# Kernel tuning notes

Hardware: AMD Instinct MI355X
Metric: run time of the kernel (lower is better)

The kernel has to match this reference:

```python
import jax, jax.numpy as jnp
import numpy as np

BITS = 8
NUM_HEADS = 16
EMB = 1024
MLP = 4096
BATCH = 4
SEQ = 1024


def _fq(x, bits, signed=True, narrow=False):
    """Fake-quantize with per-tensor absmax scale (brevitas MinMax/MaxStats style),
    straight-through-estimator round. signed+narrow => weight quant; signed non-narrow
    => activation quant; unsigned => QuantReLU output."""
    if signed:
        qmax = 2.0 ** (bits - 1) - 1.0
        qmin = -qmax if narrow else -(qmax + 1.0)
    else:
        qmax = 2.0 ** bits - 1.0
        qmin = 0.0
    scale = jax.lax.stop_gradient(jnp.max(jnp.abs(x)) / qmax)
    scale = jnp.maximum(scale, jnp.asarray(1e-8, x.dtype))
    q = x / scale
    q = q + jax.lax.stop_gradient(jnp.round(q) - q)  # STE round
    return jnp.clip(q, qmin, qmax) * scale


def _layernorm(x, eps=1e-5):
    mu = jnp.mean(x, axis=-1, keepdims=True)
    var = jnp.mean(jnp.square(x - mu), axis=-1, keepdims=True)
    return (x - mu) * jax.lax.rsqrt(var + eps)


def setup_inputs() -> dict:
    key = jax.random.key(0)
    ks = jax.random.split(key, 11)
    def w(k, shape, fan_in):
        return jax.random.normal(k, shape, jnp.float32) * (1.0 / np.sqrt(fan_in))
    return {
        "x": jax.random.normal(ks[0], (BATCH, SEQ, EMB), jnp.float32),
        "Wq": w(ks[1], (EMB, EMB), EMB), "bq": jnp.zeros((EMB,), jnp.float32),
        "Wk": w(ks[2], (EMB, EMB), EMB), "bk": jnp.zeros((EMB,), jnp.float32),
        "Wv": w(ks[3], (EMB, EMB), EMB), "bv": jnp.zeros((EMB,), jnp.float32),
        "Wo": w(ks[4], (EMB, EMB), EMB), "bo": jnp.zeros((EMB,), jnp.float32),
        "W1": w(ks[5], (MLP, EMB), EMB), "b1": jnp.zeros((MLP,), jnp.float32),
        "W2": w(ks[6], (EMB, MLP), MLP), "b2": jnp.zeros((EMB,), jnp.float32),
    }


def reference(x, Wq, bq, Wk, bk, Wv, bv, Wo, bo, W1, b1, W2, b2):
    B, S, E = x.shape
    H, D = NUM_HEADS, EMB // NUM_HEADS
    fqw = lambda W: _fq(W, BITS, signed=True, narrow=True)   # weight quant
    fqb = lambda b: _fq(b, BITS, signed=True)                # bias quant
    fqa = lambda a: _fq(a, BITS, signed=True)                # act quant

    # sdp_input_quant
    qx = fqa(x)
    # separate (unpacked) in-projections, torch Linear: y = x @ W.T + b
    q = qx @ fqw(Wq).T + fqb(bq)
    k = qx @ fqw(Wk).T + fqb(bk)
    v = qx @ fqw(Wv).T + fqb(bv)
    # [B,H,S,D]
    q = q.reshape(B, S, H, D).transpose(0, 2, 1, 3)
    k = k.reshape(B, S, H, D).transpose(0, 2, 1, 3)
    v = v.reshape(B, S, H, D).transpose(0, 2, 1, 3)

    q_scaled = fqa(q * (1.0 / np.sqrt(D)))          # q_scaled_quant
    k_t = fqa(k.transpose(0, 1, 3, 2))              # k_transposed_quant
    v = fqa(v)                                      # v_quant

    scores = jnp.einsum('bhqd,bhdk->bhqk', q_scaled, k_t)
    scores = fqa(scores)                            # softmax_input_quant
    attn = jax.nn.softmax(scores, axis=-1)
    attn = fqa(attn)                                # attn_output_weights_quant

    ctx = jnp.einsum('bhqk,bhkd->bhqd', attn, v)
    ctx = ctx.transpose(0, 2, 1, 3).reshape(B, S, E)
    ctx = fqa(ctx)                                  # out_proj_input_quant
    attn_out = ctx @ fqw(Wo).T + fqb(bo)

    # residual_sdp (QuantEltwiseAdd input quant on both operands) + layer-norm
    h = _layernorm(fqa(x) + fqa(attn_out))

    # MLP: QuantIdentity -> QuantLinear -> QuantReLU(unsigned) -> QuantLinear
    m = fqa(h)
    m = m @ fqw(W1).T + fqb(b1)
    m = _fq(jax.nn.relu(m), BITS, signed=False)
    m = m @ fqw(W2).T + fqb(b2)

    return _layernorm(fqa(h) + fqa(m))
```

## Files before the change

kernel.cpp:

```cpp
#include <hip/hip_runtime.h>
#include <cstdint>
#include <cstddef>

#define TB_B 4
#define TB_S 1024
#define TB_E 1024
#define TB_H 16
#define TB_D 64
#define TB_MLP 4096
#define TB_ROWS (TB_B * TB_S)

typedef int int4v __attribute__((ext_vector_type(4)));

#define LGKM0() __asm__ volatile("s_waitcnt lgkmcnt(0)" ::: "memory")
#define CMEMBAR() __asm__ volatile("" ::: "memory")
#define RAW_BARRIER() do { __asm__ volatile("" ::: "memory"); \
  __builtin_amdgcn_s_barrier(); __asm__ volatile("" ::: "memory"); } while (0)

static __device__ __forceinline__ void atomicMaxF(float* addr, float v) {
  atomicMax(reinterpret_cast<unsigned int*>(addr), __float_as_uint(v));
}

static __device__ __forceinline__ float fast_exp2(float x) {
#if __has_builtin(__builtin_amdgcn_exp2f)
  return __builtin_amdgcn_exp2f(x);
#else
  return exp2f(x);
#endif
}

static __device__ __forceinline__ void gl2lds16(const void* g, void* l) {
  __builtin_amdgcn_global_load_lds(
      (const __attribute__((address_space(1))) void*)g,
      (__attribute__((address_space(3))) void*)l, 16, 0, 0);
}

struct AMDesc { const float* p; long n4; int slot; };
struct AMBatch { AMDesc d[13]; };
__global__ __launch_bounds__(256) void absmax_multi_kernel(AMBatch bt, float* ws) {
  AMDesc d = bt.d[blockIdx.y];
  float m = 0.f;
  long stride = (long)gridDim.x * 256;
  for (long i = (long)blockIdx.x * 256 + threadIdx.x; i < d.n4; i += stride) {
    float4 v = ((const float4*)d.p)[i];
    m = fmaxf(m, fmaxf(fmaxf(fabsf(v.x), fabsf(v.y)), fmaxf(fabsf(v.z), fabsf(v.w))));
  }
#pragma unroll
  for (int o = 32; o; o >>= 1) m = fmaxf(m, __shfl_down(m, o, 64));
  __shared__ float sm[4];
  if (!(threadIdx.x & 63)) sm[threadIdx.x >> 6] = m;
  __syncthreads();
  if (threadIdx.x == 0)
    atomicMaxF(ws + d.slot, fmaxf(fmaxf(sm[0], sm[1]), fmaxf(sm[2], sm[3])));
}

struct QMDesc { const float* in; signed char* out; long n4; int slot; float qmin; };
struct QMBatch { QMDesc d[7]; };
__global__ __launch_bounds__(256) void quant8_multi_kernel(QMBatch bt, const float* ws) {
  QMDesc d = bt.d[blockIdx.y];
  float scale = fmaxf(ws[d.slot] / 127.f, 1e-8f);
  long stride = (long)gridDim.x * 256;
  for (long i = (long)blockIdx.x * 256 + threadIdx.x; i < d.n4; i += stride) {
    float4 v = ((const float4*)d.in)[i];
    char4 o;
    o.x = (signed char)(int)fminf(fmaxf(rintf(v.x / scale), d.qmin), 127.f);
    o.y = (signed char)(int)fminf(fmaxf(rintf(v.y / scale), d.qmin), 127.f);
    o.z = (signed char)(int)fminf(fmaxf(rintf(v.z / scale), d.qmin), 127.f);
    o.w = (signed char)(int)fminf(fmaxf(rintf(v.w / scale), d.qmin), 127.f);
    ((char4*)d.out)[i] = o;
  }
}

struct BDesc { const float* in; float* out; int n4; int slot; };
struct BBatch { BDesc d[6]; };
__global__ __launch_bounds__(256) void bias_quant_multi_kernel(BBatch bt, const float* ws) {
  BDesc d = bt.d[blockIdx.y];
  float scale = fmaxf(ws[d.slot] / 127.f, 1e-8f);
  int i = blockIdx.x * 256 + threadIdx.x;
  if (i < d.n4) {
    float4 v = ((const float4*)d.in)[i];
    float4 o;
    o.x = fminf(fmaxf(rintf(v.x / scale), -128.f), 127.f) * scale;
    o.y = fminf(fmaxf(rintf(v.y / scale), -128.f), 127.f) * scale;
    o.z = fminf(fmaxf(rintf(v.z / scale), -128.f), 127.f) * scale;
    o.w = fminf(fmaxf(rintf(v.w / scale), -128.f), 127.f) * scale;
    ((float4*)d.out)[i] = o;
  }
}

__global__ __launch_bounds__(256) void quant8_kernel(const float* __restrict__ in,
                                                     signed char* __restrict__ out8, long n4,
                                                     const float* __restrict__ amax_p,
                                                     float pre, float qmin) {
  float scale = fmaxf(amax_p[0] * pre / 127.f, 1e-8f);
  long stride = (long)gridDim.x * 256;
  for (long i = (long)blockIdx.x * 256 + threadIdx.x; i < n4; i += stride) {
    float4 v = ((const float4*)in)[i];
    char4 o;
    o.x = (signed char)(int)fminf(fmaxf(rintf(v.x * pre / scale), qmin), 127.f);
    o.y = (signed char)(int)fminf(fmaxf(rintf(v.y * pre / scale), qmin), 127.f);
    o.z = (signed char)(int)fminf(fmaxf(rintf(v.z * pre / scale), qmin), 127.f);
    o.w = (signed char)(int)fminf(fmaxf(rintf(v.w * pre / scale), qmin), 127.f);
    ((char4*)out8)[i] = o;
  }
}

__global__ __launch_bounds__(256) void relu_quant8_kernel(const float* __restrict__ in,
                                                          signed char* __restrict__ out8, long n4,
                                                          const float* __restrict__ amax_p) {
  float scale = fmaxf(amax_p[0] / 255.f, 1e-8f);
  long stride = (long)gridDim.x * 256;
  for (long i = (long)blockIdx.x * 256 + threadIdx.x; i < n4; i += stride) {
    float4 v = ((const float4*)in)[i];
    char4 o;
    o.x = (signed char)((int)fminf(fmaxf(rintf(fmaxf(v.x, 0.f) / scale), 0.f), 255.f) - 128);
    o.y = (signed char)((int)fminf(fmaxf(rintf(fmaxf(v.y, 0.f) / scale), 0.f), 255.f) - 128);
    o.z = (signed char)((int)fminf(fmaxf(rintf(fmaxf(v.z, 0.f) / scale), 0.f), 255.f) - 128);
    o.w = (signed char)((int)fminf(fmaxf(rintf(fmaxf(v.w, 0.f) / scale), 0.f), 255.f) - 128);
    ((char4*)out8)[i] = o;
  }
}

__global__ __launch_bounds__(256) void rowsum_i8_kernel(const signed char* __restrict__ w8,
                                                        int* __restrict__ out, int Kdim) {
  const int row = blockIdx.x, t = threadIdx.x;
  const signed char* p = w8 + (long)row * Kdim;
  int s = 0;
  for (int i = t * 16; i < Kdim; i += 4096) {
    int4v v = *(const int4v*)(p + i);
    const signed char* b = (const signed char*)&v;
#pragma unroll
    for (int j = 0; j < 16; j++) s += b[j];
  }
#pragma unroll
  for (int o = 32; o; o >>= 1) s += __shfl_down(s, o, 64);
  __shared__ int sm[4];
  if (!(t & 63)) sm[t >> 6] = s;
  __syncthreads();
  if (t == 0) out[row] = sm[0] + sm[1] + sm[2] + sm[3];
}

__global__ __launch_bounds__(256) void gemm_i8_kernel(
    const signed char* __restrict__ A, const signed char* __restrict__ Bw,
    const float* __restrict__ biasq,
    const float* __restrict__ amax_a, float div_a,
    const float* __restrict__ amax_b,
    const int* __restrict__ rowsum,
    float* __restrict__ C, int M, int N, int K,
    float* __restrict__ amax_out, int relu_amax, int mode) {
  __shared__ signed char As[3][8192];
  __shared__ signed char Bs[3][8192];
  const int t = threadIdx.x;
  int bx, by;
  {
    int lin = blockIdx.y * gridDim.x + blockIdx.x;
    if ((gridDim.y & 7) == 0) {
      int xcd = lin & 7, j = lin >> 3;
      bx = j % gridDim.x;
      by = (gridDim.y >> 3) * xcd + j / gridDim.x;
    } else { bx = blockIdx.x; by = blockIdx.y; }
  }
  const int m0 = by * 128, n0 = bx * 128;
  const int w = t >> 6, lane = t & 63;
  const int fr = lane & 15, quad = lane >> 4;
  const int wm = w >> 1, wn = w & 1;
  const int r0 = t >> 2;
  const int csrc = (((t & 3) ^ ((t >> 3) & 3)) << 4);
  const int sx = ((quad ^ ((fr >> 1) & 3)) << 4);

  int4v acc[4][4];
#pragma unroll
  for (int r = 0; r < 4; r++)
#pragma unroll
    for (int c = 0; c < 4; c++) acc[r][c] = (int4v){0, 0, 0, 0};

  const long arow0 = (long)(m0 + r0) * K + csrc;
  const long arow1 = (long)(m0 + r0 + 64) * K + csrc;
  const long brow0 = (long)(n0 + r0) * K + csrc;
  const long brow1 = (long)(n0 + r0 + 64) * K + csrc;

  auto stage = [&](int buf, int kt) {
    const int kk = kt << 6;
    gl2lds16(A + arow0 + kk, As[buf] + t * 16);
    gl2lds16(A + arow1 + kk, As[buf] + t * 16 + 4096);
    gl2lds16(Bw + brow0 + kk, Bs[buf] + t * 16);
    gl2lds16(Bw + brow1 + kk, Bs[buf] + t * 16 + 4096);
  };
  auto compute = [&](int buf) {
    int4v af[4], bf[4];
#pragma unroll
    for (int r = 0; r < 4; r++)
      af[r] = *(const int4v*)(As[buf] + (wm * 64 + r * 16 + fr) * 64 + sx);
#pragma unroll
    for (int c = 0; c < 4; c++)
      bf[c] = *(const int4v*)(Bs[buf] + (wn * 64 + c * 16 + fr) * 64 + sx);
#pragma unroll
    for (int r = 0; r < 4; r++)
#pragma unroll
      for (int c = 0; c < 4; c++)
        acc[r][c] = __builtin_amdgcn_mfma_i32_16x16x64_i8(af[r], bf[c], acc[r][c], 0, 0, 0);
  };

  const int nt = K >> 6;
  stage(0, 0);
  stage(1, 1);
  int cbuf = 0, sbuf = 2;
  for (int kt = 0; kt < nt - 1; ++kt) {
    __asm__ volatile("s_waitcnt vmcnt(4)" ::: "memory");
    RAW_BARRIER();
    if (kt + 2 < nt) { stage(sbuf, kt + 2); sbuf = (sbuf == 2) ? 0 : sbuf + 1; }
    compute(cbuf);
    cbuf = (cbuf == 2) ? 0 : cbuf + 1;
  }
  __asm__ volatile("s_waitcnt vmcnt(0)" ::: "memory");
  RAW_BARRIER();
  compute(cbuf);

  const int seg = (mode == 1) ? (n0 >> 10) : 0;
  const float s_a = fmaxf(amax_a[0] / div_a, 1e-8f);
  const float s_b = fmaxf(amax_b[seg] / 127.f, 1e-8f);
  const float s = s_a * s_b;
  float lmax = 0.f;
#pragma unroll
  for (int r = 0; r < 4; r++) {
    int rbase = m0 + wm * 64 + r * 16 + quad * 4;
#pragma unroll
    for (int c = 0; c < 4; c++) {
      int col = n0 + wn * 64 + c * 16 + fr;
      int corr = rowsum ? (rowsum[col] << 7) : 0;
      float bi = biasq[col];
      if (mode == 1) {
        int h = (col >> 6) & 15, dd = col & 63;
        float* cbase = C + (long)seg * ((long)TB_ROWS * TB_E);
#pragma unroll
        for (int g = 0; g < 4; g++) {
          int m = rbase + g;
          int b = m >> 10, sdx = m & 1023;
          float o = (float)acc[r][c][g] * s + bi;
          lmax = fmaxf(lmax, fabsf(o));
          cbase[((((long)b * TB_H + h) * TB_S) + sdx) * TB_D + dd] = o;
        }
      } else {
#pragma unroll
        for (int g = 0; g < 4; g++) {
          float o = (float)(acc[r][c][g] + corr) * s + bi;
          lmax = fmaxf(lmax, relu_amax ? fmaxf(o, 0.f) : fabsf(o));
          C[(long)(rbase + g) * N + col] = o;
        }
      }
    }
  }
#pragma unroll
  for (int o = 32; o; o >>= 1) lmax = fmaxf(lmax, __shfl_down(lmax, o, 64));
  __shared__ float redm[4];
  if (!lane) redm[w] = lmax;
  __syncthreads();
  if (t == 0) atomicMaxF(amax_out + seg, fmaxf(fmaxf(redm[0], redm[1]), fmaxf(redm[2], redm[3])));
}

__global__ __launch_bounds__(256) void quant8_vb_kernel(const float* __restrict__ v,
                                                        const float* __restrict__ amax_p,
                                                        signed char* __restrict__ v8b) {
  __shared__ signed char tile[64][80];
  const int bh = blockIdx.x;
  const int jb = blockIdx.y;
  const int s0 = jb * 64;
  const int t = threadIdx.x;
  const float scale = fmaxf(amax_p[0] / 127.f, 1e-8f);
#pragma unroll
  for (int it = 0; it < 4; it++) {
    int idx = t + it * 256;
    int r = idx >> 4, c4 = (idx & 15) * 4;
    float4 vv = *(const float4*)(v + ((long)bh * TB_S + s0 + r) * TB_D + c4);
    tile[c4 + 0][r] = (signed char)(int)fminf(fmaxf(rintf(vv.x / scale), -128.f), 127.f);
    tile[c4 + 1][r] = (signed char)(int)fminf(fmaxf(rintf(vv.y / scale), -128.f), 127.f);
    tile[c4 + 2][r] = (signed char)(int)fminf(fmaxf(rintf(vv.z / scale), -128.f), 127.f);
    tile[c4 + 3][r] = (signed char)(int)fminf(fmaxf(rintf(vv.w / scale), -128.f), 127.f);
  }
  __syncthreads();
  int d = t >> 2, sb = (t & 3) * 16;
  int4v o = *(const int4v*)&tile[d][sb];
  *(int4v*)(v8b + (((long)bh * 16 + jb) * 64 + d) * 64 + sb) = o;
}

__global__ __launch_bounds__(256) void attn_rowmax_kernel(const signed char* __restrict__ q8,
                                                          const signed char* __restrict__ k8,
                                                          int* __restrict__ irowmax,
                                                          int* __restrict__ imax_out) {
  const int bh = blockIdx.x;
  const int t = threadIdx.x, w = t >> 6, lane = t & 63;
  const int fr = lane & 15, quad = lane >> 4;
  const int i0 = blockIdx.y * 64 + w * 16;
  const long base = (long)bh * TB_S;
  int4v qf = *(const int4v*)(q8 + (base + i0 + fr) * 64 + quad * 16);
  int mx = -2147483647, mn = 2147483647;
  for (int j0 = 0; j0 < TB_S; j0 += 16) {
    int4v kf = *(const int4v*)(k8 + (base + j0 + fr) * 64 + quad * 16);
    int4v sc = __builtin_amdgcn_mfma_i32_16x16x64_i8(kf, qf, (int4v){0, 0, 0, 0}, 0, 0, 0);
    mx = max(mx, max(max(sc[0], sc[1]), max(sc[2], sc[3])));
    mn = min(mn, min(min(sc[0], sc[1]), min(sc[2], sc[3])));
  }
  mx = max(mx, __shfl_xor(mx, 16, 64));
  mx = max(mx, __shfl_xor(mx, 32, 64));
  mn = min(mn, __shfl_xor(mn, 16, 64));
  mn = min(mn, __shfl_xor(mn, 32, 64));
  if (quad == 0) irowmax[(long)bh * TB_S + i0 + fr] = mx;
  int gm = max(mx, -mn);
#pragma unroll
  for (int o = 32; o; o >>= 1) gm = max(gm, __shfl_down(gm, o, 64));
  __shared__ int sm[4];
  if (!lane) sm[w] = gm;
  __syncthreads();
  if (t == 0) atomicMax(imax_out, max(max(sm[0], sm[1]), max(sm[2], sm[3])));
}

__global__ __launch_bounds__(256) void attn_rowsum_kernel(
    const signed char* __restrict__ q8, const signed char* __restrict__ k8,
    const int* __restrict__ irowmax, const int* __restrict__ imax_p,
    const float* __restrict__ amax_q, const float* __restrict__ amax_k,
    float* __restrict__ rowl, float* __restrict__ amax_attn) {
  const int bh = blockIdx.x;
  const int t = threadIdx.x, w = t >> 6, lane = t & 63;
  const int fr = lane & 15, quad = lane >> 4;
  const int i0 = blockIdx.y * 64 + w * 16;
  const float s_q = fmaxf(amax_q[0] * 0.125f / 127.f, 1e-8f);
  const float s_k = fmaxf(amax_k[0] / 127.f, 1e-8f);
  const float sqk = s_q * s_k;
  const float s_sc = fmaxf((float)imax_p[0] * sqk / 127.f, 1e-8f);
  const float c1 = sqk / s_sc;
  const float aa = s_sc * 1.44269504088896340736f;
  const long base = (long)bh * TB_S;
  int4v qf = *(const int4v*)(q8 + (base + i0 + fr) * 64 + quad * 16);
  const int imr = irowmax[base + i0 + fr];
  const float qmax = fminf(fmaxf(rintf((float)imr * c1), -128.f), 127.f);
  const float qa = qmax * aa;
  float l = 0.f;
  for (int j0 = 0; j0 < TB_S; j0 += 16) {
    int4v kf = *(const int4v*)(k8 + (base + j0 + fr) * 64 + quad * 16);
    int4v sc = __builtin_amdgcn_mfma_i32_16x16x64_i8(kf, qf, (int4v){0, 0, 0, 0}, 0, 0, 0);
#pragma unroll
    for (int g = 0; g < 4; g++) {
      float qv = fminf(fmaxf(rintf((float)sc[g] * c1), -128.f), 127.f);
      l += fast_exp2(fmaf(qv, aa, -qa));
    }
  }
  l += __shfl_xor(l, 16, 64);
  l += __shfl_xor(l, 32, 64);
  if (quad == 0) rowl[base + i0 + fr] = l;
  float inv = 1.f / l;
#pragma unroll
  for (int o = 32; o; o >>= 1) inv = fmaxf(inv, __shfl_down(inv, o, 64));
  __shared__ float smf[4];
  if (!lane) smf[w] = inv;
  __syncthreads();
  if (t == 0) atomicMaxF(amax_attn, fmaxf(fmaxf(smf[0], smf[1]), fmaxf(smf[2], smf[3])));
}

__global__ __launch_bounds__(256) void attn_pv_kernel(
    const signed char* __restrict__ q8, const signed char* __restrict__ k8,
    const signed char* __restrict__ v8b,
    const int* __restrict__ irowmax, const int* __restrict__ imax_p,
    const float* __restrict__ amax_q, const float* __restrict__ amax_k,
    const float* __restrict__ amax_v, const float* __restrict__ amax_attn,
    const float* __restrict__ rowl,
    float* __restrict__ ctx, float* __restrict__ amax_ctx) {
  __shared__ signed char latt[4][16][80];
  const int bh = blockIdx.x, b = bh >> 4, h = bh & 15;
  const int t = threadIdx.x, w = t >> 6, lane = t & 63;
  const int fr = lane & 15, quad = lane >> 4;
  const int i0 = blockIdx.y * 64 + w * 16;
  const float s_q = fmaxf(amax_q[0] * 0.125f / 127.f, 1e-8f);
  const float s_k = fmaxf(amax_k[0] / 127.f, 1e-8f);
  const float sqk = s_q * s_k;
  const float s_sc = fmaxf((float)imax_p[0] * sqk / 127.f, 1e-8f);
  const float c1 = sqk / s_sc;
  const float aa = s_sc * 1.44269504088896340736f;
  const float s_v = fmaxf(amax_v[0] / 127.f, 1e-8f);
  const float s_at = fmaxf(amax_attn[0] / 127.f, 1e-8f);
  const long base = (long)bh * TB_S;
  int4v qf = *(const int4v*)(q8 + (base + i0 + fr) * 64 + quad * 16);
  const int imr = irowmax[base + i0 + fr];
  const float qmax = fminf(fmaxf(rintf((float)imr * c1), -128.f), 127.f);
  const float bexp = qmax * aa;
  const float li = rowl[base + i0 + fr];
  const float invls = 1.f / (li * s_at);
  int4v accv[4];
#pragma unroll
  for (int dtile = 0; dtile < 4; dtile++) accv[dtile] = (int4v){0, 0, 0, 0};

  for (int j0 = 0; j0 < TB_S; j0 += 64) {
#pragma unroll
    for (int tt = 0; tt < 4; tt++) {
      int4v kf = *(const int4v*)(k8 + (base + j0 + tt * 16 + fr) * 64 + quad * 16);
      int4v sc = __builtin_amdgcn_mfma_i32_16x16x64_i8(kf, qf, (int4v){0, 0, 0, 0}, 0, 0, 0);
      int packed = 0;
#pragma unroll
      for (int g = 0; g < 4; g++) {
        float qv = fminf(fmaxf(rintf((float)sc[g] * c1), -128.f), 127.f);
        float e = fast_exp2(fmaf(qv, aa, -bexp));
        int code = (int)fminf(fmaxf(rintf(e * invls), -128.f), 127.f);
        packed |= (code & 255) << (g * 8);
      }
      *(int*)&latt[w][fr][tt * 16 + quad * 4] = packed;
    }
    LGKM0();
    int4v af = *(const int4v*)&latt[w][fr][quad * 16];
    const signed char* vbase = v8b + (((long)bh * 16 + (j0 >> 6)) * 64) * 64;
#pragma unroll
    for (int dtile = 0; dtile < 4; dtile++) {
      int4v vf = *(const int4v*)(vbase + (dtile * 16 + fr) * 64 + quad * 16);
      accv[dtile] = __builtin_amdgcn_mfma_i32_16x16x64_i8(af, vf, accv[dtile], 0, 0, 0);
    }
    CMEMBAR();
  }
  const float sav = s_at * s_v;
  float cmax = 0.f;
#pragma unroll
  for (int dtile = 0; dtile < 4; dtile++) {
#pragma unroll
    for (int g = 0; g < 4; g++) {
      float val = (float)accv[dtile][g] * sav;
      cmax = fmaxf(cmax, fabsf(val));
      int irow = i0 + quad * 4 + g;
      ctx[(((long)(b * TB_S + irow)) * TB_H + h) * TB_D + dtile * 16 + fr] = val;
    }
  }
#pragma unroll
  for (int o = 32; o; o >>= 1) cmax = fmaxf(cmax, __shfl_down(cmax, o, 64));
  __shared__ float smf[4];
  if (!lane) smf[w] = cmax;
  __syncthreads();
  if (t == 0) atomicMaxF(amax_ctx, fmaxf(fmaxf(smf[0], smf[1]), fmaxf(smf[2], smf[3])));
}

__global__ __launch_bounds__(256) void resid_ln_kernel(const signed char* __restrict__ a8,
                                                       const float* __restrict__ amax_a,
                                                       const float* __restrict__ braw,
                                                       const float* __restrict__ amax_b,
                                                       float* __restrict__ outp,
                                                       float* __restrict__ amax_out) {
  const int t = threadIdx.x, w = t >> 6, lane = t & 63;
  const int row = blockIdx.x * 4 + w;
  const float sa = fmaxf(amax_a[0] / 127.f, 1e-8f);
  const float sb = fmaxf(amax_b[0] / 127.f, 1e-8f);
  const long base = (long)row * TB_E;
  float v[16];
  float s = 0.f, q = 0.f;
#pragma unroll
  for (int j = 0; j < 4; j++) {
    char4 a = ((const char4*)(a8 + base))[j * 64 + lane];
    float4 bv = *(const float4*)(braw + base + j * 256 + lane * 4);
    float x0 = (float)a.x * sa + fminf(fmaxf(rintf(bv.x / sb), -128.f), 127.f) * sb;
    float x1 = (float)a.y * sa + fminf(fmaxf(rintf(bv.y / sb), -128.f), 127.f) * sb;
    float x2 = (float)a.z * sa + fminf(fmaxf(rintf(bv.z / sb), -128.f), 127.f) * sb;
    float x3 = (float)a.w * sa + fminf(fmaxf(rintf(bv.w / sb), -128.f), 127.f) * sb;
    v[j * 4 + 0] = x0; v[j * 4 + 1] = x1; v[j * 4 + 2] = x2; v[j * 4 + 3] = x3;
    s += (x0 + x1) + (x2 + x3);
    q += (x0 * x0 + x1 * x1) + (x2 * x2 + x3 * x3);
  }
#pragma unroll
  for (int o = 32; o; o >>= 1) {
    s += __shfl_xor(s, o, 64);
    q += __shfl_xor(q, o, 64);
  }
  const float mu = s * (1.f / TB_E);
  const float var = fmaxf(q * (1.f / TB_E) - mu * mu, 0.f);
  const float rs = 1.f / sqrtf(var + 1e-5f);
  float lm = 0.f;
#pragma unroll
  for (int j = 0; j < 4; j++) {
    float4 o4;
    o4.x = (v[j * 4 + 0] - mu) * rs;
    o4.y = (v[j * 4 + 1] - mu) * rs;
    o4.z = (v[j * 4 + 2] - mu) * rs;
    o4.w = (v[j * 4 + 3] - mu) * rs;
    *(float4*)(outp + base + j * 256 + lane * 4) = o4;
    lm = fmaxf(lm, fmaxf(fmaxf(fabsf(o4.x), fabsf(o4.y)), fmaxf(fabsf(o4.z), fabsf(o4.w))));
  }
#pragma unroll
  for (int o = 32; o; o >>= 1) lm = fmaxf(lm, __shfl_down(lm, o, 64));
  __shared__ float redm[4];
  if (!lane) redm[w] = lm;
  __syncthreads();
  if (t == 0) atomicMaxF(amax_out, fmaxf(fmaxf(redm[0], redm[1]), fmaxf(redm[2], redm[3])));
}

#define SL_X 0
#define SL_WQ 1
#define SL_WK 2
#define SL_WV 3
#define SL_WO 4
#define SL_W1 5
#define SL_W2 6
#define SL_BQ 7
#define SL_BK 8
#define SL_BV 9
#define SL_BO 10
#define SL_B1 11
#define SL_B2 12
#define SL_Q 13
#define SL_K 14
#define SL_V 15
#define SL_SCI 16
#define SL_ATTN 17
#define SL_CTX 18
#define SL_AO 19
#define SL_H 20
#define SL_RELU 21
#define SL_M2 22
#define SL_DUMMY 23

static inline int nblocks(long n) {
  long b = (n + 255) / 256;
  return (int)(b > 2048 ? 2048 : b);
}

extern "C" void kernel_launch(void* const* d_in, const int* in_sizes, int n_in,
                              void* d_out, int out_size, void* d_ws, size_t ws_size,
                              hipStream_t stream) {
  const float* x  = (const float*)d_in[0];
  const float* Wq = (const float*)d_in[1];
  const float* bq = (const float*)d_in[2];
  const float* Wk = (const float*)d_in[3];
  const float* bk = (const float*)d_in[4];
  const float* Wv = (const float*)d_in[5];
  const float* bv = (const float*)d_in[6];
  const float* Wo = (const float*)d_in[7];
  const float* bo = (const float*)d_in[8];
  const float* W1 = (const float*)d_in[9];
  const float* b1 = (const float*)d_in[10];
  const float* W2 = (const float*)d_in[11];
  const float* b2 = (const float*)d_in[12];
  float* ws = (float*)d_ws;
  float* out = (float*)d_out;

  const long SZ_XE = (long)TB_ROWS * TB_E;
  const long SZ_W  = (long)TB_E * TB_E;
  const long SZ_M1 = (long)TB_ROWS * TB_MLP;

  const long OFF_QBQ = 1024, OFF_QBK = 2048, OFF_QBV = 3072, OFF_QBO = 4096;
  const long OFF_QB1 = 5120, OFF_QB2 = 9216;
  const long OFF_RSUM = 10240;
  const long OFF_Q  = 65536;
  const long OFF_K  = OFF_Q + SZ_XE;
  const long OFF_V  = OFF_K + SZ_XE;
  const long OFF_M2 = OFF_V + SZ_XE;
  const long OFF_IRM = OFF_M2 + SZ_XE;
  const long OFF_ROWL = OFF_IRM + 65536;
  const long OFF_M1 = OFF_ROWL + 65536;
  const long OFF_I8 = OFF_M1 + SZ_M1;

  float* qbuf = ws + OFF_Q;  float* kbuf = ws + OFF_K;  float* vbuf = ws + OFF_V;
  float* m2   = ws + OFF_M2;
  int*   irowmax = (int*)(ws + OFF_IRM);
  float* rowl = ws + OFF_ROWL;
  float* m1 = ws + OFF_M1;
  float* ctx = qbuf;
  float* attn_out = kbuf;
  float* hbuf = vbuf;
  float* qbq_ = ws + OFF_QBQ; float* qbk_ = ws + OFF_QBK;
  float* qbv_ = ws + OFF_QBV; float* qbo_ = ws + OFF_QBO;
  float* qb1_ = ws + OFF_QB1; float* qb2_ = ws + OFF_QB2;
  int* rsum = (int*)(ws + OFF_RSUM);
  int* imax = (int*)(ws + SL_SCI);

  signed char* i8base = (signed char*)(ws + OFF_I8);
  signed char* qx8  = i8base;
  signed char* wq8  = qx8 + SZ_XE;
  signed char* wk8  = wq8 + SZ_W;
  signed char* wv8  = wk8 + SZ_W;
  signed char* wo8  = wv8 + SZ_W;
  signed char* w18  = wo8 + SZ_W;
  signed char* w28  = w18 + SZ_XE;
  signed char* ctx8 = w28 + SZ_XE;
  signed char* m08  = ctx8 + SZ_XE;
  signed char* m18  = m08 + SZ_XE;
  signed char* q8   = m18 + SZ_M1;
  signed char* k8   = q8 + SZ_XE;
  signed char* v8b  = k8 + SZ_XE;

  hipMemsetAsync(ws, 0, 4096, stream);

  AMBatch am;
  am.d[0]  = {x,  SZ_XE/4, SL_X};
  am.d[1]  = {Wq, SZ_W/4,  SL_WQ};
  am.d[2]  = {Wk, SZ_W/4,  SL_WK};
  am.d[3]  = {Wv, SZ_W/4,  SL_WV};
  am.d[4]  = {Wo, SZ_W/4,  SL_WO};
  am.d[5]  = {W1, SZ_XE/4, SL_W1};
  am.d[6]  = {W2, SZ_XE/4, SL_W2};
  am.d[7]  = {bq, 256,     SL_BQ};
  am.d[8]  = {bk, 256,     SL_BK};
  am.d[9]  = {bv, 256,     SL_BV};
  am.d[10] = {bo, 256,     SL_BO};
  am.d[11] = {b1, 1024,    SL_B1};
  am.d[12] = {b2, 256,     SL_B2};
  absmax_multi_kernel<<<dim3(64, 13), 256, 0, stream>>>(am, ws);

  QMBatch qm;
  qm.d[0] = {x,  qx8, SZ_XE/4, SL_X,  -128.f};
  qm.d[1] = {Wq, wq8, SZ_W/4,  SL_WQ, -127.f};
  qm.d[2] = {Wk, wk8, SZ_W/4,  SL_WK, -127.f};
  qm.d[3] = {Wv, wv8, SZ_W/4,  SL_WV, -127.f};
  qm.d[4] = {W1, w18, SZ_XE/4, SL_W1, -127.f};
  qm.d[5] = {W2, w28, SZ_XE/4, SL_W2, -127.f};
  qm.d[6] = {Wo, wo8, SZ_W/4,  SL_WO, -127.f};
  quant8_multi_kernel<<<dim3(64, 7), 256, 0, stream>>>(qm, ws);
  rowsum_i8_kernel<<<TB_E, 256, 0, stream>>>(w28, rsum, TB_MLP);
  BBatch bb;
  bb.d[0] = {bq, qbq_, 256,  SL_BQ};
  bb.d[1] = {bk, qbk_, 256,  SL_BK};
  bb.d[2] = {bv, qbv_, 256,  SL_BV};
  bb.d[3] = {bo, qbo_, 256,  SL_BO};
  bb.d[4] = {b1, qb1_, 1024, SL_B1};
  bb.d[5] = {b2, qb2_, 256,  SL_B2};
  bias_quant_multi_kernel<<<dim3(4, 6), 256, 0, stream>>>(bb, ws);

  gemm_i8_kernel<<<dim3(3*TB_E/128, TB_ROWS/128), 256, 0, stream>>>(
      qx8, wq8, qbq_, ws + SL_X, 127.f, ws + SL_WQ, nullptr, qbuf,
      TB_ROWS, 3*TB_E, TB_E, ws + SL_Q, 0, 1);

  quant8_kernel<<<2048, 256, 0, stream>>>(qbuf, q8, SZ_XE/4, ws + SL_Q, 0.125f, -128.f);
  quant8_kernel<<<2048, 256, 0, stream>>>(kbuf, k8, SZ_XE/4, ws + SL_K, 1.f, -128.f);
  quant8_vb_kernel<<<dim3(TB_B*TB_H, TB_S/64), 256, 0, stream>>>(vbuf, ws + SL_V, v8b);

  attn_rowmax_kernel<<<dim3(TB_B*TB_H, TB_S/64), 256, 0, stream>>>(q8, k8, irowmax, imax);
  attn_rowsum_kernel<<<dim3(TB_B*TB_H, TB_S/64), 256, 0, stream>>>(
      q8, k8, irowmax, imax, ws + SL_Q, ws + SL_K, rowl, ws + SL_ATTN);
  attn_pv_kernel<<<dim3(TB_B*TB_H, TB_S/64), 256, 0, stream>>>(
      q8, k8, v8b, irowmax, imax, ws + SL_Q, ws + SL_K, ws + SL_V, ws + SL_ATTN,
      rowl, ctx, ws + SL_CTX);

  quant8_kernel<<<2048, 256, 0, stream>>>(ctx, ctx8, SZ_XE/4, ws + SL_CTX, 1.f, -128.f);
  gemm_i8_kernel<<<dim3(TB_E/128, TB_ROWS/128), 256, 0, stream>>>(
      ctx8, wo8, qbo_, ws + SL_CTX, 127.f, ws + SL_WO, nullptr, attn_out,
      TB_ROWS, TB_E, TB_E, ws + SL_AO, 0, 0);

  resid_ln_kernel<<<TB_ROWS/4, 256, 0, stream>>>(qx8, ws + SL_X, attn_out, ws + SL_AO, hbuf, ws + SL_H);

  quant8_kernel<<<2048, 256, 0, stream>>>(hbuf, m08, SZ_XE/4, ws + SL_H, 1.f, -128.f);
  gemm_i8_kernel<<<dim3(TB_MLP/128, TB_ROWS/128), 256, 0, stream>>>(
      m08, w18, qb1_, ws + SL_H, 127.f, ws + SL_W1, nullptr, m1,
      TB_ROWS, TB_MLP, TB_E, ws + SL_RELU, 1, 0);
  relu_quant8_kernel<<<nblocks(SZ_M1/4), 256, 0, stream>>>(m1, m18, SZ_M1/4, ws + SL_RELU);
  gemm_i8_kernel<<<dim3(TB_E/128, TB_ROWS/128), 256, 0, stream>>>(
      m18, w28, qb2_, ws + SL_RELU, 255.f, ws + SL_W2, rsum, m2,
      TB_ROWS, TB_E, TB_MLP, ws + SL_M2, 0, 0);

  resid_ln_kernel<<<TB_ROWS/4, 256, 0, stream>>>(m08, ws + SL_H, m2, ws + SL_M2, out, ws + SL_DUMMY);
}
```

Baseline: 468.6 us.

## Split K across two warp groups in int8 GEMM with 512-thread blocks

The int8 GEMM now runs 8 waves per block. Two groups of four waves each handle half of a 128-wide K step, and their partial accumulators are reduced through shared memory before the epilogue. The pipeline goes from triple-buffered 64-wide K tiles to double-buffered 128-wide tiles, with an extra barrier after each compute. The aim is more waves to hide latency and fewer loop iterations, at the cost of 64KB of LDS per block, an added reduction step, and lower occupancy in blocks per CU.

```diff
diff --git a/kernel.cpp b/kernel.cpp
--- a/kernel.cpp
+++ b/kernel.cpp
@@ -140,7 +140,7 @@
   if (t == 0) out[row] = sm[0] + sm[1] + sm[2] + sm[3];
 }
 
-__global__ __launch_bounds__(256) void gemm_i8_kernel(
+__global__ __launch_bounds__(512, 4) void gemm_i8_kernel(
     const signed char* __restrict__ A, const signed char* __restrict__ Bw,
     const float* __restrict__ biasq,
     const float* __restrict__ amax_a, float div_a,
@@ -148,8 +148,8 @@
     const int* __restrict__ rowsum,
     float* __restrict__ C, int M, int N, int K,
     float* __restrict__ amax_out, int relu_amax, int mode) {
-  __shared__ signed char As[3][8192];
-  __shared__ signed char Bs[3][8192];
+  __shared__ signed char smem[65536];
+  __shared__ float redm[4];
   const int t = threadIdx.x;
   int bx, by;
   {
@@ -163,37 +163,43 @@
   const int m0 = by * 128, n0 = bx * 128;
   const int w = t >> 6, lane = t & 63;
   const int fr = lane & 15, quad = lane >> 4;
-  const int wm = w >> 1, wn = w & 1;
+  const int kg = w >> 2;
+  const int wm = (w >> 1) & 1, wn = w & 1;
   const int r0 = t >> 2;
   const int csrc = (((t & 3) ^ ((t >> 3) & 3)) << 4);
   const int sx = ((quad ^ ((fr >> 1) & 3)) << 4);
 
+  signed char* Asm = smem;
+  signed char* Bsm = smem + 32768;
+
   int4v acc[4][4];
 #pragma unroll
   for (int r = 0; r < 4; r++)
 #pragma unroll
     for (int c = 0; c < 4; c++) acc[r][c] = (int4v){0, 0, 0, 0};
 
-  const long arow0 = (long)(m0 + r0) * K + csrc;
-  const long arow1 = (long)(m0 + r0 + 64) * K + csrc;
-  const long brow0 = (long)(n0 + r0) * K + csrc;
-  const long brow1 = (long)(n0 + r0 + 64) * K + csrc;
+  const long arow = (long)(m0 + r0) * K + csrc;
+  const long brow = (long)(n0 + r0) * K + csrc;
 
   auto stage = [&](int buf, int kt) {
-    const int kk = kt << 6;
-    gl2lds16(A + arow0 + kk, As[buf] + t * 16);
-    gl2lds16(A + arow1 + kk, As[buf] + t * 16 + 4096);
-    gl2lds16(Bw + brow0 + kk, Bs[buf] + t * 16);
-    gl2lds16(Bw + brow1 + kk, Bs[buf] + t * 16 + 4096);
+    const int kk = kt << 7;
+    signed char* ad = Asm + buf * 16384 + t * 16;
+    signed char* bd = Bsm + buf * 16384 + t * 16;
+    gl2lds16(A + arow + kk, ad);
+    gl2lds16(A + arow + kk + 64, ad + 8192);
+    gl2lds16(Bw + brow + kk, bd);
+    gl2lds16(Bw + brow + kk + 64, bd + 8192);
   };
   auto compute = [&](int buf) {
+    const signed char* ab = Asm + buf * 16384 + kg * 8192;
+    const signed char* bb = Bsm + buf * 16384 + kg * 8192;
     int4v af[4], bf[4];
 #pragma unroll
     for (int r = 0; r < 4; r++)
-      af[r] = *(const int4v*)(As[buf] + (wm * 64 + r * 16 + fr) * 64 + sx);
+      af[r] = *(const int4v*)(ab + (wm * 64 + r * 16 + fr) * 64 + sx);
 #pragma unroll
     for (int c = 0; c < 4; c++)
-      bf[c] = *(const int4v*)(Bs[buf] + (wn * 64 + c * 16 + fr) * 64 + sx);
+      bf[c] = *(const int4v*)(bb + (wn * 64 + c * 16 + fr) * 64 + sx);
 #pragma unroll
     for (int r = 0; r < 4; r++)
 #pragma unroll
@@ -201,61 +207,89 @@
         acc[r][c] = __builtin_amdgcn_mfma_i32_16x16x64_i8(af[r], bf[c], acc[r][c], 0, 0, 0);
   };
 
-  const int nt = K >> 6;
+  const int nt = K >> 7;
   stage(0, 0);
-  stage(1, 1);
-  int cbuf = 0, sbuf = 2;
-  for (int kt = 0; kt < nt - 1; ++kt) {
-    __asm__ volatile("s_waitcnt vmcnt(4)" ::: "memory");
+  int buf = 0;
+  for (int kt = 0; kt < nt; ++kt) {
+    if (kt + 1 < nt) {
+      stage(buf ^ 1, kt + 1);
+      __asm__ volatile("s_waitcnt vmcnt(4)" ::: "memory");
+    } else {
+      __asm__ volatile("s_waitcnt vmcnt(0)" ::: "memory");
+    }
     RAW_BARRIER();
-    if (kt + 2 < nt) { stage(sbuf, kt + 2); sbuf = (sbuf == 2) ? 0 : sbuf + 1; }
-    compute(cbuf);
-    cbuf = (cbuf == 2) ? 0 : cbuf + 1;
-  }
-  __asm__ volatile("s_waitcnt vmcnt(0)" ::: "memory");
-  RAW_BARRIER();
-  compute(cbuf);
-
-  const int seg = (mode == 1) ? (n0 >> 10) : 0;
-  const float s_a = fmaxf(amax_a[0] / div_a, 1e-8f);
-  const float s_b = fmaxf(amax_b[seg] / 127.f, 1e-8f);
-  const float s = s_a * s_b;
-  float lmax = 0.f;
-#pragma unroll
-  for (int r = 0; r < 4; r++) {
-    int rbase = m0 + wm * 64 + r * 16 + quad * 4;
-#pragma unroll
-    for (int c = 0; c < 4; c++) {
-      int col = n0 + wn * 64 + c * 16 + fr;
-      int corr = rowsum ? (rowsum[col] << 7) : 0;
-      float bi = biasq[col];
-      if (mode == 1) {
-        int h = (col >> 6) & 15, dd = col & 63;
-        float* cbase = C + (long)seg * ((long)TB_ROWS * TB_E);
-#pragma unroll
-        for (int g = 0; g < 4; g++) {
-          int m = rbase + g;
-          int b = m >> 10, sdx = m & 1023;
-          float o = (float)acc[r][c][g] * s + bi;
-          lmax = fmaxf(lmax, fabsf(o));
-          cbase[((((long)b * TB_H + h) * TB_S) + sdx) * TB_D + dd] = o;
+    compute(buf);
+    RAW_BARRIER();
+    buf ^= 1;
+  }
+
+  {
+    int4v* mb = (int4v*)smem;
+    const int bi = (w & 3) * 64 + lane;
+    if (kg == 1) {
+#pragma unroll
+      for (int r = 0; r < 4; r++)
+#pragma unroll
+        for (int c = 0; c < 4; c++)
+          mb[(r * 4 + c) * 256 + bi] = acc[r][c];
+    }
+    __syncthreads();
+    if (kg == 0) {
+#pragma unroll
+      for (int r = 0; r < 4; r++)
+#pragma unroll
+        for (int c = 0; c < 4; c++) {
+          int4v p = mb[(r * 4 + c) * 256 + bi];
+          acc[r][c][0] += p[0]; acc[r][c][1] += p[1];
+          acc[r][c][2] += p[2]; acc[r][c][3] += p[3];
         }
-      } else {
-#pragma unroll
-        for (int g = 0; g < 4; g++) {
-          float o = (float)(acc[r][c][g] + corr) * s + bi;
-          lmax = fmaxf(lmax, relu_amax ? fmaxf(o, 0.f) : fabsf(o));
-          C[(long)(rbase + g) * N + col] = o;
+    }
+  }
+
+  if (kg == 0) {
+    const int seg = (mode == 1) ? (n0 >> 10) : 0;
+    const float s_a = fmaxf(amax_a[0] / div_a, 1e-8f);
+    const float s_b = fmaxf(amax_b[seg] / 127.f, 1e-8f);
+    const float s = s_a * s_b;
+    float lmax = 0.f;
+#pragma unroll
+    for (int r = 0; r < 4; r++) {
+      int rbase = m0 + wm * 64 + r * 16 + quad * 4;
+#pragma unroll
+      for (int c = 0; c < 4; c++) {
+        int col = n0 + wn * 64 + c * 16 + fr;
+        int corr = rowsum ? (rowsum[col] << 7) : 0;
+        float bi = biasq[col];
+        if (mode == 1) {
+          int h = (col >> 6) & 15, dd = col & 63;
+          float* cbase = C + (long)seg * ((long)TB_ROWS * TB_E);
+#pragma unroll
+          for (int g = 0; g < 4; g++) {
+            int m = rbase + g;
+            int b = m >> 10, sdx = m & 1023;
+            float o = (float)acc[r][c][g] * s + bi;
+            lmax = fmaxf(lmax, fabsf(o));
+            cbase[((((long)b * TB_H + h) * TB_S) + sdx) * TB_D + dd] = o;
+          }
+        } else {
+#pragma unroll
+          for (int g = 0; g < 4; g++) {
+            float o = (float)(acc[r][c][g] + corr) * s + bi;
+            lmax = fmaxf(lmax, relu_amax ? fmaxf(o, 0.f) : fabsf(o));
+            C[(long)(rbase + g) * N + col] = o;
+          }
         }
       }
     }
-  }
-#pragma unroll
-  for (int o = 32; o; o >>= 1) lmax = fmaxf(lmax, __shfl_down(lmax, o, 64));
-  __shared__ float redm[4];
-  if (!lane) redm[w] = lmax;
-  __syncthreads();
-  if (t == 0) atomicMaxF(amax_out + seg, fmaxf(fmaxf(redm[0], redm[1]), fmaxf(redm[2], redm[3])));
+#pragma unroll
+    for (int o = 32; o; o >>= 1) lmax = fmaxf(lmax, __shfl_down(lmax, o, 64));
+    if (!lane) redm[w] = lmax;
+  }
+  __syncthreads();
+  if (t == 0) {
+    const int seg = (mode == 1) ? (n0 >> 10) : 0;
+    atomicMaxF(amax_out + seg, fmaxf(fmaxf(redm[0], redm[1]), fmaxf(redm[2], redm[3])));
+  }
 }
 
 __global__ __launch_bounds__(256) void quant8_vb_kernel(const float* __restrict__ v,
@@ -616,7 +650,7 @@
   bb.d[5] = {b2, qb2_, 256,  SL_B2};
   bias_quant_multi_kernel<<<dim3(4, 6), 256, 0, stream>>>(bb, ws);
 
-  gemm_i8_kernel<<<dim3(3*TB_E/128, TB_ROWS/128), 256, 0, stream>>>(
+  gemm_i8_kernel<<<dim3(3*TB_E/128, TB_ROWS/128), 512, 0, stream>>>(
       qx8, wq8, qbq_, ws + SL_X, 127.f, ws + SL_WQ, nullptr, qbuf,
       TB_ROWS, 3*TB_E, TB_E, ws + SL_Q, 0, 1);
 
@@ -632,18 +666,18 @@
       rowl, ctx, ws + SL_CTX);
 
   quant8_kernel<<<2048, 256, 0, stream>>>(ctx, ctx8, SZ_XE/4, ws + SL_CTX, 1.f, -128.f);
-  gemm_i8_kernel<<<dim3(TB_E/128, TB_ROWS/128), 256, 0, stream>>>(
+  gemm_i8_kernel<<<dim3(TB_E/128, TB_ROWS/128), 512, 0, stream>>>(
       ctx8, wo8, qbo_, ws + SL_CTX, 127.f, ws + SL_WO, nullptr, attn_out,
       TB_ROWS, TB_E, TB_E, ws + SL_AO, 0, 0);
 
   resid_ln_kernel<<<TB_ROWS/4, 256, 0, stream>>>(qx8, ws + SL_X, attn_out, ws + SL_AO, hbuf, ws + SL_H);
 
   quant8_kernel<<<2048, 256, 0, stream>>>(hbuf, m08, SZ_XE/4, ws + SL_H, 1.f, -128.f);
-  gemm_i8_kernel<<<dim3(TB_MLP/128, TB_ROWS/128), 256, 0, stream>>>(
+  gemm_i8_kernel<<<dim3(TB_MLP/128, TB_ROWS/128), 512, 0, stream>>>(
       m08, w18, qb1_, ws + SL_H, 127.f, ws + SL_W1, nullptr, m1,
       TB_ROWS, TB_MLP, TB_E, ws + SL_RELU, 1, 0);
   relu_quant8_kernel<<<nblocks(SZ_M1/4), 256, 0, stream>>>(m1, m18, SZ_M1/4, ws + SL_RELU);
-  gemm_i8_kernel<<<dim3(TB_E/128, TB_ROWS/128), 256, 0, stream>>>(
+  gemm_i8_kernel<<<dim3(TB_E/128, TB_ROWS/128), 512, 0, stream>>>(
       m18, w28, qb2_, ws + SL_RELU, 255.f, ws + SL_W2, rsum, m2,
       TB_ROWS, TB_E, TB_MLP, ws + SL_M2, 0, 0);
 
```

Result: slower. 482.2 us (+2.9%).

## Use 512-thread blocks with double buffering in the int8 GEMM kernel

Applied to the files above, without the earlier changes.

Doubles the threads per block in the int8 MFMA GEMM to 8 waves, so each wave computes a 32x64 sub-tile instead of 64x64. This halves the accumulators per wave and lets each thread issue half as many loads per stage. The LDS pipeline drops from a three-buffer, two-tiles-ahead prefetch to a two-buffer scheme with a second barrier per k-step. The aim is more waves in flight and lower register pressure, at the cost of shallower prefetch, extra synchronisation and less data reuse per wave.

```diff
diff --git a/kernel.cpp b/kernel.cpp
--- a/kernel.cpp
+++ b/kernel.cpp
@@ -140,7 +140,7 @@
   if (t == 0) out[row] = sm[0] + sm[1] + sm[2] + sm[3];
 }
 
-__global__ __launch_bounds__(256) void gemm_i8_kernel(
+__global__ __launch_bounds__(512, 2) void gemm_i8_kernel(
     const signed char* __restrict__ A, const signed char* __restrict__ Bw,
     const float* __restrict__ biasq,
     const float* __restrict__ amax_a, float div_a,
@@ -148,8 +148,9 @@
     const int* __restrict__ rowsum,
     float* __restrict__ C, int M, int N, int K,
     float* __restrict__ amax_out, int relu_amax, int mode) {
-  __shared__ signed char As[3][8192];
-  __shared__ signed char Bs[3][8192];
+  __shared__ signed char Asm[2][8192];
+  __shared__ signed char Bsm[2][8192];
+  __shared__ float redm[8];
   const int t = threadIdx.x;
   int bx, by;
   {
@@ -168,34 +169,30 @@
   const int csrc = (((t & 3) ^ ((t >> 3) & 3)) << 4);
   const int sx = ((quad ^ ((fr >> 1) & 3)) << 4);
 
-  int4v acc[4][4];
-#pragma unroll
-  for (int r = 0; r < 4; r++)
+  int4v acc[2][4];
+#pragma unroll
+  for (int r = 0; r < 2; r++)
 #pragma unroll
     for (int c = 0; c < 4; c++) acc[r][c] = (int4v){0, 0, 0, 0};
 
-  const long arow0 = (long)(m0 + r0) * K + csrc;
-  const long arow1 = (long)(m0 + r0 + 64) * K + csrc;
-  const long brow0 = (long)(n0 + r0) * K + csrc;
-  const long brow1 = (long)(n0 + r0 + 64) * K + csrc;
+  const long arow = (long)(m0 + r0) * K + csrc;
+  const long brow = (long)(n0 + r0) * K + csrc;
 
   auto stage = [&](int buf, int kt) {
     const int kk = kt << 6;
-    gl2lds16(A + arow0 + kk, As[buf] + t * 16);
-    gl2lds16(A + arow1 + kk, As[buf] + t * 16 + 4096);
-    gl2lds16(Bw + brow0 + kk, Bs[buf] + t * 16);
-    gl2lds16(Bw + brow1 + kk, Bs[buf] + t * 16 + 4096);
+    gl2lds16(A + arow + kk, Asm[buf] + t * 16);
+    gl2lds16(Bw + brow + kk, Bsm[buf] + t * 16);
   };
   auto compute = [&](int buf) {
-    int4v af[4], bf[4];
-#pragma unroll
-    for (int r = 0; r < 4; r++)
-      af[r] = *(const int4v*)(As[buf] + (wm * 64 + r * 16 + fr) * 64 + sx);
+    int4v af[2], bf[4];
+#pragma unroll
+    for (int r = 0; r < 2; r++)
+      af[r] = *(const int4v*)(Asm[buf] + (wm * 32 + r * 16 + fr) * 64 + sx);
 #pragma unroll
     for (int c = 0; c < 4; c++)
-      bf[c] = *(const int4v*)(Bs[buf] + (wn * 64 + c * 16 + fr) * 64 + sx);
-#pragma unroll
-    for (int r = 0; r < 4; r++)
+      bf[c] = *(const int4v*)(Bsm[buf] + (wn * 64 + c * 16 + fr) * 64 + sx);
+#pragma unroll
+    for (int r = 0; r < 2; r++)
 #pragma unroll
       for (int c = 0; c < 4; c++)
         acc[r][c] = __builtin_amdgcn_mfma_i32_16x16x64_i8(af[r], bf[c], acc[r][c], 0, 0, 0);
@@ -203,18 +200,19 @@
 
   const int nt = K >> 6;
   stage(0, 0);
-  stage(1, 1);
-  int cbuf = 0, sbuf = 2;
-  for (int kt = 0; kt < nt - 1; ++kt) {
-    __asm__ volatile("s_waitcnt vmcnt(4)" ::: "memory");
+  int buf = 0;
+  for (int kt = 0; kt < nt; ++kt) {
+    if (kt + 1 < nt) {
+      stage(buf ^ 1, kt + 1);
+      __asm__ volatile("s_waitcnt vmcnt(2)" ::: "memory");
+    } else {
+      __asm__ volatile("s_waitcnt vmcnt(0)" ::: "memory");
+    }
     RAW_BARRIER();
-    if (kt + 2 < nt) { stage(sbuf, kt + 2); sbuf = (sbuf == 2) ? 0 : sbuf + 1; }
-    compute(cbuf);
-    cbuf = (cbuf == 2) ? 0 : cbuf + 1;
-  }
-  __asm__ volatile("s_waitcnt vmcnt(0)" ::: "memory");
-  RAW_BARRIER();
-  compute(cbuf);
+    compute(buf);
+    RAW_BARRIER();
+    buf ^= 1;
+  }
 
   const int seg = (mode == 1) ? (n0 >> 10) : 0;
   const float s_a = fmaxf(amax_a[0] / div_a, 1e-8f);
@@ -222,8 +220,8 @@
   const float s = s_a * s_b;
   float lmax = 0.f;
 #pragma unroll
-  for (int r = 0; r < 4; r++) {
-    int rbase = m0 + wm * 64 + r * 16 + quad * 4;
+  for (int r = 0; r < 2; r++) {
+    int rbase = m0 + wm * 32 + r * 16 + quad * 4;
 #pragma unroll
     for (int c = 0; c < 4; c++) {
       int col = n0 + wn * 64 + c * 16 + fr;
@@ -252,10 +250,13 @@
   }
 #pragma unroll
   for (int o = 32; o; o >>= 1) lmax = fmaxf(lmax, __shfl_down(lmax, o, 64));
-  __shared__ float redm[4];
   if (!lane) redm[w] = lmax;
   __syncthreads();
-  if (t == 0) atomicMaxF(amax_out + seg, fmaxf(fmaxf(redm[0], redm[1]), fmaxf(redm[2], redm[3])));
+  if (t == 0) {
+    float m01 = fmaxf(fmaxf(redm[0], redm[1]), fmaxf(redm[2], redm[3]));
+    float m23 = fmaxf(fmaxf(redm[4], redm[5]), fmaxf(redm[6], redm[7]));
+    atomicMaxF(amax_out + seg, fmaxf(m01, m23));
+  }
 }
 
 __global__ __launch_bounds__(256) void quant8_vb_kernel(const float* __restrict__ v,
@@ -616,7 +617,7 @@
   bb.d[5] = {b2, qb2_, 256,  SL_B2};
   bias_quant_multi_kernel<<<dim3(4, 6), 256, 0, stream>>>(bb, ws);
 
-  gemm_i8_kernel<<<dim3(3*TB_E/128, TB_ROWS/128), 256, 0, stream>>>(
+  gemm_i8_kernel<<<dim3(3*TB_E/128, TB_ROWS/128), 512, 0, stream>>>(
       qx8, wq8, qbq_, ws + SL_X, 127.f, ws + SL_WQ, nullptr, qbuf,
       TB_ROWS, 3*TB_E, TB_E, ws + SL_Q, 0, 1);
 
@@ -632,18 +633,18 @@
       rowl, ctx, ws + SL_CTX);
 
   quant8_kernel<<<2048, 256, 0, stream>>>(ctx, ctx8, SZ_XE/4, ws + SL_CTX, 1.f, -128.f);
-  gemm_i8_kernel<<<dim3(TB_E/128, TB_ROWS/128), 256, 0, stream>>>(
+  gemm_i8_kernel<<<dim3(TB_E/128, TB_ROWS/128), 512, 0, stream>>>(
       ctx8, wo8, qbo_, ws + SL_CTX, 127.f, ws + SL_WO, nullptr, attn_out,
       TB_ROWS, TB_E, TB_E, ws + SL_AO, 0, 0);
 
   resid_ln_kernel<<<TB_ROWS/4, 256, 0, stream>>>(qx8, ws + SL_X, attn_out, ws + SL_AO, hbuf, ws + SL_H);
 
   quant8_kernel<<<2048, 256, 0, stream>>>(hbuf, m08, SZ_XE/4, ws + SL_H, 1.f, -128.f);
-  gemm_i8_kernel<<<dim3(TB_MLP/128, TB_ROWS/128), 256, 0, stream>>>(
+  gemm_i8_kernel<<<dim3(TB_MLP/128, TB_ROWS/128), 512, 0, stream>>>(
       m08, w18, qb1_, ws + SL_H, 127.f, ws + SL_W1, nullptr, m1,
       TB_ROWS, TB_MLP, TB_E, ws + SL_RELU, 1, 0);
   relu_quant8_kernel<<<nblocks(SZ_M1/4), 256, 0, stream>>>(m1, m18, SZ_M1/4, ws + SL_RELU);
-  gemm_i8_kernel<<<dim3(TB_E/128, TB_ROWS/128), 256, 0, stream>>>(
+  gemm_i8_kernel<<<dim3(TB_E/128, TB_ROWS/128), 512, 0, stream>>>(
       m18, w28, qb2_, ws + SL_RELU, 255.f, ws + SL_W2, rsum, m2,
       TB_ROWS, TB_E, TB_MLP, ws + SL_M2, 0, 0);
 
```

Result: no change. 459.5 us (-1.9%).
